# Kernel optimization log

Measured on AMD Instinct MI355X. Metric: run time of the kernel, lower is better.

Reference implementation:

```python
import jax, jax.numpy as jnp
import numpy as np

NUM_LAYERS = 4
INPUT_DIM = 512
BATCH = 16384


def setup_inputs() -> dict:
    key = jax.random.key(0)
    kx, kw, kb = jax.random.split(key, 3)
    x = jax.random.normal(kx, (BATCH, INPUT_DIM), dtype=jnp.float32)
    # PyTorch nn.Linear init: U(-1/sqrt(fan_in), 1/sqrt(fan_in))
    bound = 1.0 / np.sqrt(INPUT_DIM)
    W = jax.random.uniform(kw, (NUM_LAYERS, INPUT_DIM, INPUT_DIM), jnp.float32, -bound, bound)
    b = jax.random.uniform(kb, (NUM_LAYERS, INPUT_DIM), jnp.float32, -bound, bound)
    return {"x": x, "W": W, "b": b}


def reference(x, W, b):
    # x: [B, D]; W: [L, D, D] (torch Linear weight, so y = x @ W_i.T + b_i)
    x_list = [x]
    for i in range(NUM_LAYERS):
        x_ = x_list[-1]
        # sequentially accumulate dot-product residuals against all prior activations
        for x_pre in x_list[:-1]:
            s = jnp.sum(x_ * x_pre, axis=-1, keepdims=True)  # [B, 1]
            x_ = x_ + s
        y = jnp.einsum("bd,ed->be", x_, W[i]) + b[i]  # Linear: x_ @ W_i.T + b_i
        x_list.append(y)
    out = jnp.concatenate(x_list[1:], axis=-1)  # [B, L*D]
    return out
```

## Files before the change

kernel.cpp:

```cpp
#include <hip/hip_runtime.h>
#include <stdint.h>


#define BROWS 16384
#define DIM 512
#define NL 4
#define OUTSTRIDE (NL * DIM)

#define BM 128
#define BN 128
#define BK 32

typedef unsigned short ushort_t;
typedef __attribute__((ext_vector_type(8))) short bf16x8;
typedef __attribute__((ext_vector_type(4))) float f32x4;

__device__ inline ushort_t f32_to_bf16(float f) {
    union { float f; uint32_t u; } v; v.f = f;
    uint32_t u = v.u;
    uint32_t r = (u + 0x7fffu + ((u >> 16) & 1u)) >> 16;
    return (ushort_t)r;
}

__device__ inline float bf16_bits_to_f32(ushort_t u) {
    union { uint32_t u; float f; } v; v.u = ((uint32_t)u) << 16; return v.f;
}

__device__ inline float wave_reduce_sum(float v) {
    #pragma unroll
    for (int off = 32; off > 0; off >>= 1) v += __shfl_down(v, off, 64);
    return v;
}

__global__ __launch_bounds__(256) void convw_kernel(
    const float* __restrict__ W, ushort_t* __restrict__ Wb,
    float* __restrict__ wsum)
{
    int row = blockIdx.x;
    int t = threadIdx.x;
    const float* wp = W + (size_t)row * DIM;
    float f0 = wp[2 * t], f1 = wp[2 * t + 1];
    ushort_t* wbp = Wb + (size_t)row * DIM;
    wbp[2 * t]     = f32_to_bf16(f0);
    wbp[2 * t + 1] = f32_to_bf16(f1);
    __shared__ float red[4];
    int wave = t >> 6, lane = t & 63;
    float r = wave_reduce_sum(f0 + f1);
    if (lane == 0) red[wave] = r;
    __syncthreads();
    if (t == 0) wsum[row] = red[0] + red[1] + red[2] + red[3];
}

__global__ __launch_bounds__(256) void conv0_kernel(
    const float* __restrict__ x0, ushort_t* __restrict__ xb0,
    float* __restrict__ sums)
{
    int wave = threadIdx.x >> 6, lane = threadIdx.x & 63;
    int b = blockIdx.x * 4 + wave;
    const float* xp = x0 + (size_t)b * DIM + lane * 8;
    float4 a = ((const float4*)xp)[0];
    float4 c4 = ((const float4*)xp)[1];
    float f[8] = {a.x, a.y, a.z, a.w, c4.x, c4.y, c4.z, c4.w};
    bf16x8 o;
    float s = 0.f;
    #pragma unroll
    for (int i = 0; i < 8; ++i) {
        o[i] = (short)f32_to_bf16(f[i]);
        s += f[i];
    }
    *(bf16x8*)(xb0 + (size_t)b * DIM + lane * 8) = o;
    s = wave_reduce_sum(s);
    if (lane == 0) sums[b] = s;
}

__global__ __launch_bounds__(256) void dots_kernel(
    const ushort_t* __restrict__ xb, float* __restrict__ sums,
    float* __restrict__ cvals, int lp1)
{
    int wave = threadIdx.x >> 6, lane = threadIdx.x & 63;
    int b = blockIdx.x * 4 + wave;
    bf16x8 v = *(const bf16x8*)(xb + ((size_t)lp1 * BROWS + b) * DIM + lane * 8);
    float xi[8];
    float ssum = 0.f;
    #pragma unroll
    for (int i = 0; i < 8; ++i) {
        xi[i] = bf16_bits_to_f32((ushort_t)v[i]);
        ssum += xi[i];
    }
    float dots[3] = {0.f, 0.f, 0.f};
    #pragma unroll
    for (int j = 0; j < 3; ++j) {
        if (j < lp1) {
            bf16x8 w = *(const bf16x8*)(xb + ((size_t)j * BROWS + b) * DIM + lane * 8);
            float d = 0.f;
            #pragma unroll
            for (int i = 0; i < 8; ++i)
                d += xi[i] * bf16_bits_to_f32((ushort_t)w[i]);
            dots[j] = d;
        }
    }
    ssum = wave_reduce_sum(ssum);
    #pragma unroll
    for (int j = 0; j < 3; ++j)
        dots[j] = wave_reduce_sum(dots[j]);
    if (lane == 0) {
        sums[lp1 * BROWS + b] = ssum;
        float c = 0.f;
        for (int j = 0; j < lp1; ++j)
            c = c + dots[j] + c * sums[j * BROWS + b];
        cvals[lp1 * BROWS + b] = c;
    }
}

__global__ __launch_bounds__(256) void gemm_kernel(
    const ushort_t* __restrict__ A,
    const ushort_t* __restrict__ Wb,
    const float* __restrict__ bias,
    const float* __restrict__ wsum,
    const float* __restrict__ cvals,
    float* __restrict__ out,
    ushort_t* __restrict__ xb_next)
{
    __shared__ __align__(16) ushort_t sA[BM * BK];
    __shared__ __align__(16) ushort_t sB[BN * BK];

    int tid  = threadIdx.x;
    int wave = tid >> 6;
    int lane = tid & 63;
    int wm = wave >> 1, wn = wave & 1;
    int bm = blockIdx.y * BM;
    int bn = blockIdx.x * BN;

    f32x4 acc[4][4] = {};

    int srow = lane >> 2;
    int scol = (lane & 3) * 8;

    for (int k0 = 0; k0 < DIM; k0 += BK) {
        __syncthreads();
        #pragma unroll
        for (int t2 = 0; t2 < 2; ++t2) {
            int r = wave * 32 + t2 * 16;
            const ushort_t* gA = A  + (size_t)(bm + r + srow) * DIM + k0 + scol;
            const ushort_t* gB = Wb + (size_t)(bn + r + srow) * DIM + k0 + scol;
            __builtin_amdgcn_global_load_lds(
                (const __attribute__((address_space(1))) void*)gA,
                (__attribute__((address_space(3))) void*)(sA + r * BK), 16, 0, 0);
            __builtin_amdgcn_global_load_lds(
                (const __attribute__((address_space(1))) void*)gB,
                (__attribute__((address_space(3))) void*)(sB + r * BK), 16, 0, 0);
        }
        __syncthreads();

        int q = lane >> 4;
        int rr = lane & 15;
        bf16x8 af[4], bfr[4];
        #pragma unroll
        for (int mi = 0; mi < 4; ++mi)
            af[mi] = *(const bf16x8*)(sA + (wm * 64 + mi * 16 + rr) * BK + q * 8);
        #pragma unroll
        for (int ni = 0; ni < 4; ++ni)
            bfr[ni] = *(const bf16x8*)(sB + (wn * 64 + ni * 16 + rr) * BK + q * 8);
        #pragma unroll
        for (int mi = 0; mi < 4; ++mi)
            #pragma unroll
            for (int ni = 0; ni < 4; ++ni)
                acc[mi][ni] = __builtin_amdgcn_mfma_f32_16x16x32_bf16(
                    af[mi], bfr[ni], acc[mi][ni], 0, 0, 0);
    }

    int q = lane >> 4, nlane = lane & 15;
    #pragma unroll
    for (int ni = 0; ni < 4; ++ni) {
        int n_g = bn + wn * 64 + ni * 16 + nlane;
        float ws = wsum[n_g];
        float bs = bias[n_g];
        #pragma unroll
        for (int mi = 0; mi < 4; ++mi) {
            int m_base = bm + wm * 64 + mi * 16 + q * 4;
            #pragma unroll
            for (int r = 0; r < 4; ++r) {
                int m_g = m_base + r;
                float c = cvals ? cvals[m_g] : 0.f;
                float v = acc[mi][ni][r] + c * ws + bs;
                out[(size_t)m_g * OUTSTRIDE + n_g] = v;
                if (xb_next)
                    xb_next[(size_t)m_g * DIM + n_g] = f32_to_bf16(v);
            }
        }
    }
}

extern "C" void kernel_launch(void* const* d_in, const int* in_sizes, int n_in,
                              void* d_out, int out_size, void* d_ws, size_t ws_size,
                              hipStream_t stream) {
    (void)in_sizes; (void)n_in; (void)out_size; (void)ws_size;
    const float* x0   = (const float*)d_in[0];
    const float* W    = (const float*)d_in[1];
    const float* bias = (const float*)d_in[2];
    float* out = (float*)d_out;

    char* ws = (char*)d_ws;
    ushort_t* xb   = (ushort_t*)ws;
    ushort_t* Wb   = (ushort_t*)(ws + 67108864);
    float*    wsum = (float*)   (ws + 69206016);
    float*    sums = (float*)   (ws + 69214208);
    float*    cvals= (float*)   (ws + 69476352);

    convw_kernel<<<NL * DIM, 256, 0, stream>>>(W, Wb, wsum);
    conv0_kernel<<<BROWS / 4, 256, 0, stream>>>(x0, xb, sums);

    dim3 ggrid(DIM / BN, BROWS / BM);
    for (int l = 0; l < NL; ++l) {
        gemm_kernel<<<ggrid, 256, 0, stream>>>(
            xb + (size_t)l * BROWS * DIM,
            Wb + (size_t)l * DIM * DIM,
            bias + l * DIM,
            wsum + l * DIM,
            (l > 0) ? (cvals + l * BROWS) : nullptr,
            out + l * DIM,
            (l < NL - 1) ? (xb + (size_t)(l + 1) * BROWS * DIM) : nullptr);
        if (l < NL - 1)
            dots_kernel<<<BROWS / 4, 256, 0, stream>>>(xb, sums, cvals, l + 1);
    }
}
```

Before: 302.8 us.

## Fuse dot-product reductions into GEMM epilogue, double-buffer LDS, merge prep kernels

```diff
diff --git a/kernel.cpp b/kernel.cpp
--- a/kernel.cpp
+++ b/kernel.cpp
@@ -10,6 +10,7 @@
 #define BM 128
 #define BN 128
 #define BK 32
+#define NT (DIM / BK)
 
 typedef unsigned short ushort_t;
 typedef __attribute__((ext_vector_type(8))) short bf16x8;
@@ -32,160 +33,191 @@
     return v;
 }
 
-__global__ __launch_bounds__(256) void convw_kernel(
-    const float* __restrict__ W, ushort_t* __restrict__ Wb,
-    float* __restrict__ wsum)
+__global__ __launch_bounds__(256) void prep_kernel(
+    const float* __restrict__ W, const float* __restrict__ x0,
+    ushort_t* __restrict__ Wb, float* __restrict__ wsum,
+    ushort_t* __restrict__ xb0, float* __restrict__ sum0)
 {
-    int row = blockIdx.x;
     int t = threadIdx.x;
-    const float* wp = W + (size_t)row * DIM;
-    float f0 = wp[2 * t], f1 = wp[2 * t + 1];
-    ushort_t* wbp = Wb + (size_t)row * DIM;
-    wbp[2 * t]     = f32_to_bf16(f0);
-    wbp[2 * t + 1] = f32_to_bf16(f1);
-    __shared__ float red[4];
     int wave = t >> 6, lane = t & 63;
-    float r = wave_reduce_sum(f0 + f1);
-    if (lane == 0) red[wave] = r;
-    __syncthreads();
-    if (t == 0) wsum[row] = red[0] + red[1] + red[2] + red[3];
-}
-
-__global__ __launch_bounds__(256) void conv0_kernel(
-    const float* __restrict__ x0, ushort_t* __restrict__ xb0,
-    float* __restrict__ sums)
-{
-    int wave = threadIdx.x >> 6, lane = threadIdx.x & 63;
-    int b = blockIdx.x * 4 + wave;
-    const float* xp = x0 + (size_t)b * DIM + lane * 8;
-    float4 a = ((const float4*)xp)[0];
-    float4 c4 = ((const float4*)xp)[1];
-    float f[8] = {a.x, a.y, a.z, a.w, c4.x, c4.y, c4.z, c4.w};
-    bf16x8 o;
-    float s = 0.f;
-    #pragma unroll
-    for (int i = 0; i < 8; ++i) {
-        o[i] = (short)f32_to_bf16(f[i]);
-        s += f[i];
-    }
-    *(bf16x8*)(xb0 + (size_t)b * DIM + lane * 8) = o;
-    s = wave_reduce_sum(s);
-    if (lane == 0) sums[b] = s;
-}
-
-__global__ __launch_bounds__(256) void dots_kernel(
-    const ushort_t* __restrict__ xb, float* __restrict__ sums,
-    float* __restrict__ cvals, int lp1)
-{
-    int wave = threadIdx.x >> 6, lane = threadIdx.x & 63;
-    int b = blockIdx.x * 4 + wave;
-    bf16x8 v = *(const bf16x8*)(xb + ((size_t)lp1 * BROWS + b) * DIM + lane * 8);
-    float xi[8];
-    float ssum = 0.f;
-    #pragma unroll
-    for (int i = 0; i < 8; ++i) {
-        xi[i] = bf16_bits_to_f32((ushort_t)v[i]);
-        ssum += xi[i];
-    }
-    float dots[3] = {0.f, 0.f, 0.f};
-    #pragma unroll
-    for (int j = 0; j < 3; ++j) {
-        if (j < lp1) {
-            bf16x8 w = *(const bf16x8*)(xb + ((size_t)j * BROWS + b) * DIM + lane * 8);
-            float d = 0.f;
-            #pragma unroll
-            for (int i = 0; i < 8; ++i)
-                d += xi[i] * bf16_bits_to_f32((ushort_t)w[i]);
-            dots[j] = d;
-        }
-    }
-    ssum = wave_reduce_sum(ssum);
-    #pragma unroll
-    for (int j = 0; j < 3; ++j)
-        dots[j] = wave_reduce_sum(dots[j]);
-    if (lane == 0) {
-        sums[lp1 * BROWS + b] = ssum;
-        float c = 0.f;
-        for (int j = 0; j < lp1; ++j)
-            c = c + dots[j] + c * sums[j * BROWS + b];
-        cvals[lp1 * BROWS + b] = c;
-    }
-}
-
+    if (blockIdx.x < NL * DIM) {
+        int row = blockIdx.x;
+        const float* wp = W + (size_t)row * DIM;
+        float f0 = wp[2 * t], f1 = wp[2 * t + 1];
+        ushort_t* wbp = Wb + (size_t)row * DIM;
+        wbp[2 * t]     = f32_to_bf16(f0);
+        wbp[2 * t + 1] = f32_to_bf16(f1);
+        __shared__ float red[4];
+        float r = wave_reduce_sum(f0 + f1);
+        if (lane == 0) red[wave] = r;
+        __syncthreads();
+        if (t == 0) wsum[row] = red[0] + red[1] + red[2] + red[3];
+    } else {
+        int b = (blockIdx.x - NL * DIM) * 4 + wave;
+        const float* xp = x0 + (size_t)b * DIM + lane * 8;
+        float4 a = ((const float4*)xp)[0];
+        float4 c4 = ((const float4*)xp)[1];
+        float f[8] = {a.x, a.y, a.z, a.w, c4.x, c4.y, c4.z, c4.w};
+        bf16x8 o;
+        float s = 0.f;
+        #pragma unroll
+        for (int i = 0; i < 8; ++i) {
+            o[i] = (short)f32_to_bf16(f[i]);
+            s += f[i];
+        }
+        *(bf16x8*)(xb0 + (size_t)b * DIM + lane * 8) = o;
+        s = wave_reduce_sum(s);
+        if (lane == 0) sum0[b] = s;
+    }
+}
+
+template <int L, bool HASNEXT>
 __global__ __launch_bounds__(256) void gemm_kernel(
-    const ushort_t* __restrict__ A,
+    const ushort_t* __restrict__ xb,
     const ushort_t* __restrict__ Wb,
     const float* __restrict__ bias,
     const float* __restrict__ wsum,
-    const float* __restrict__ cvals,
     float* __restrict__ out,
-    ushort_t* __restrict__ xb_next)
+    ushort_t* __restrict__ xb_next,
+    const float* __restrict__ sum0,
+    float* __restrict__ psum,
+    float* __restrict__ pdot)
 {
-    __shared__ __align__(16) ushort_t sA[BM * BK];
-    __shared__ __align__(16) ushort_t sB[BN * BK];
+    __shared__ __align__(16) ushort_t sA[2][BM * BK];
+    __shared__ __align__(16) ushort_t sB[2][BN * BK];
+    __shared__ float sC[BM];
 
     int tid  = threadIdx.x;
     int wave = tid >> 6;
     int lane = tid & 63;
     int wm = wave >> 1, wn = wave & 1;
-    int bm = blockIdx.y * BM;
-    int bn = blockIdx.x * BN;
+
+    int lid  = blockIdx.x;
+    int xcd  = lid & 7, slot = lid >> 3;
+    int orig = xcd * 64 + slot;
+    int bx = orig & 3, by = orig >> 2;
+    int bm = by * BM;
+    int bn = bx * BN;
+
+    const ushort_t* A = xb + (size_t)L * BROWS * DIM;
 
     f32x4 acc[4][4] = {};
 
     int srow = lane >> 2;
     int scol = (lane & 3) * 8;
-
-    for (int k0 = 0; k0 < DIM; k0 += BK) {
-        __syncthreads();
+    const ushort_t* gA0 = A  + (size_t)(bm + srow) * DIM + scol;
+    const ushort_t* gB0 = Wb + (size_t)(bn + srow) * DIM + scol;
+
+    auto stage = [&](int buf, int k0) {
         #pragma unroll
         for (int t2 = 0; t2 < 2; ++t2) {
             int r = wave * 32 + t2 * 16;
-            const ushort_t* gA = A  + (size_t)(bm + r + srow) * DIM + k0 + scol;
-            const ushort_t* gB = Wb + (size_t)(bn + r + srow) * DIM + k0 + scol;
             __builtin_amdgcn_global_load_lds(
-                (const __attribute__((address_space(1))) void*)gA,
-                (__attribute__((address_space(3))) void*)(sA + r * BK), 16, 0, 0);
+                (const __attribute__((address_space(1))) void*)(gA0 + (size_t)r * DIM + k0),
+                (__attribute__((address_space(3))) void*)(&sA[buf][r * BK]), 16, 0, 0);
             __builtin_amdgcn_global_load_lds(
-                (const __attribute__((address_space(1))) void*)gB,
-                (__attribute__((address_space(3))) void*)(sB + r * BK), 16, 0, 0);
-        }
-        __syncthreads();
-
-        int q = lane >> 4;
-        int rr = lane & 15;
+                (const __attribute__((address_space(1))) void*)(gB0 + (size_t)r * DIM + k0),
+                (__attribute__((address_space(3))) void*)(&sB[buf][r * BK]), 16, 0, 0);
+        }
+    };
+
+    stage(0, 0);
+    __syncthreads();
+
+    int q8 = (lane >> 4) * 8;
+    int rr = lane & 15;
+    for (int t = 0; t < NT; ++t) {
+        int cur = t & 1;
+        if (t + 1 < NT) stage(cur ^ 1, (t + 1) * BK);
         bf16x8 af[4], bfr[4];
         #pragma unroll
         for (int mi = 0; mi < 4; ++mi)
-            af[mi] = *(const bf16x8*)(sA + (wm * 64 + mi * 16 + rr) * BK + q * 8);
+            af[mi] = *(const bf16x8*)(&sA[cur][(wm * 64 + mi * 16 + rr) * BK + q8]);
         #pragma unroll
         for (int ni = 0; ni < 4; ++ni)
-            bfr[ni] = *(const bf16x8*)(sB + (wn * 64 + ni * 16 + rr) * BK + q * 8);
+            bfr[ni] = *(const bf16x8*)(&sB[cur][(wn * 64 + ni * 16 + rr) * BK + q8]);
         #pragma unroll
         for (int mi = 0; mi < 4; ++mi)
             #pragma unroll
             for (int ni = 0; ni < 4; ++ni)
                 acc[mi][ni] = __builtin_amdgcn_mfma_f32_16x16x32_bf16(
                     af[mi], bfr[ni], acc[mi][ni], 0, 0, 0);
+        __syncthreads();
+    }
+
+    if (L > 0) {
+        if (tid < BM) {
+            int row = bm + tid;
+            float c = 0.f;
+            #pragma unroll
+            for (int j = 0; j < L; ++j) {
+                constexpr int pb = L * (L - 1) / 2;
+                const float* pd = pdot + ((size_t)(pb + j) * 8) * BROWS + row;
+                float d = 0.f;
+                #pragma unroll
+                for (int p = 0; p < 8; ++p) d += pd[(size_t)p * BROWS];
+                float sj;
+                if (j == 0) sj = sum0[row];
+                else {
+                    const float* ps = psum + ((size_t)(j - 1) * 8) * BROWS + row;
+                    sj = 0.f;
+                    #pragma unroll
+                    for (int p = 0; p < 8; ++p) sj += ps[(size_t)p * BROWS];
+                }
+                c = c + d + c * sj;
+            }
+            sC[tid] = c;
+        }
+        __syncthreads();
     }
 
     int q = lane >> 4, nlane = lane & 15;
+    int pq = wn * 4 + bx;
+    float ws4[4], bs4[4];
     #pragma unroll
     for (int ni = 0; ni < 4; ++ni) {
         int n_g = bn + wn * 64 + ni * 16 + nlane;
-        float ws = wsum[n_g];
-        float bs = bias[n_g];
-        #pragma unroll
-        for (int mi = 0; mi < 4; ++mi) {
-            int m_base = bm + wm * 64 + mi * 16 + q * 4;
+        ws4[ni] = wsum[n_g];
+        bs4[ni] = bias[n_g];
+    }
+    #pragma unroll
+    for (int mi = 0; mi < 4; ++mi) {
+        #pragma unroll
+        for (int r = 0; r < 4; ++r) {
+            int mloc = wm * 64 + mi * 16 + q * 4 + r;
+            int m_g = bm + mloc;
+            float c = (L > 0) ? sC[mloc] : 0.f;
+            float vsum = 0.f, vdot0 = 0.f, vdot1 = 0.f, vdot2 = 0.f;
             #pragma unroll
-            for (int r = 0; r < 4; ++r) {
-                int m_g = m_base + r;
-                float c = cvals ? cvals[m_g] : 0.f;
-                float v = acc[mi][ni][r] + c * ws + bs;
+            for (int ni = 0; ni < 4; ++ni) {
+                int n_g = bn + wn * 64 + ni * 16 + nlane;
+                float v = acc[mi][ni][r] + c * ws4[ni] + bs4[ni];
                 out[(size_t)m_g * OUTSTRIDE + n_g] = v;
-                if (xb_next)
+                if constexpr (HASNEXT) {
                     xb_next[(size_t)m_g * DIM + n_g] = f32_to_bf16(v);
+                    vsum += v;
+                    vdot0 += v * bf16_bits_to_f32(xb[((size_t)0 * BROWS + m_g) * DIM + n_g]);
+                    if (L >= 1)
+                        vdot1 += v * bf16_bits_to_f32(xb[((size_t)1 * BROWS + m_g) * DIM + n_g]);
+                    if (L >= 2)
+                        vdot2 += v * bf16_bits_to_f32(xb[((size_t)2 * BROWS + m_g) * DIM + n_g]);
+                }
+            }
+            if constexpr (HASNEXT) {
+                #pragma unroll
+                for (int off = 8; off > 0; off >>= 1) {
+                    vsum  += __shfl_xor(vsum,  off, 64);
+                    vdot0 += __shfl_xor(vdot0, off, 64);
+                    if (L >= 1) vdot1 += __shfl_xor(vdot1, off, 64);
+                    if (L >= 2) vdot2 += __shfl_xor(vdot2, off, 64);
+                }
+                if (nlane == 0) {
+                    constexpr int pbn = (L + 1) * L / 2;
+                    psum[((size_t)L * 8 + pq) * BROWS + m_g] = vsum;
+                    pdot[((size_t)(pbn + 0) * 8 + pq) * BROWS + m_g] = vdot0;
+                    if (L >= 1) pdot[((size_t)(pbn + 1) * 8 + pq) * BROWS + m_g] = vdot1;
+                    if (L >= 2) pdot[((size_t)(pbn + 2) * 8 + pq) * BROWS + m_g] = vdot2;
+                }
             }
         }
     }
@@ -204,23 +236,23 @@
     ushort_t* xb   = (ushort_t*)ws;
     ushort_t* Wb   = (ushort_t*)(ws + 67108864);
     float*    wsum = (float*)   (ws + 69206016);
-    float*    sums = (float*)   (ws + 69214208);
-    float*    cvals= (float*)   (ws + 69476352);
-
-    convw_kernel<<<NL * DIM, 256, 0, stream>>>(W, Wb, wsum);
-    conv0_kernel<<<BROWS / 4, 256, 0, stream>>>(x0, xb, sums);
-
-    dim3 ggrid(DIM / BN, BROWS / BM);
-    for (int l = 0; l < NL; ++l) {
-        gemm_kernel<<<ggrid, 256, 0, stream>>>(
-            xb + (size_t)l * BROWS * DIM,
-            Wb + (size_t)l * DIM * DIM,
-            bias + l * DIM,
-            wsum + l * DIM,
-            (l > 0) ? (cvals + l * BROWS) : nullptr,
-            out + l * DIM,
-            (l < NL - 1) ? (xb + (size_t)(l + 1) * BROWS * DIM) : nullptr);
-        if (l < NL - 1)
-            dots_kernel<<<BROWS / 4, 256, 0, stream>>>(xb, sums, cvals, l + 1);
-    }
-}
+    float*    sum0 = (float*)   (ws + 69214208);
+    float*    psum = (float*)   (ws + 69279744);
+    float*    pdot = (float*)   (ws + 70852608);
+
+    prep_kernel<<<NL * DIM + BROWS / 4, 256, 0, stream>>>(W, x0, Wb, wsum, xb, sum0);
+
+    const int nblk = (BROWS / BM) * (DIM / BN);
+    gemm_kernel<0, true><<<nblk, 256, 0, stream>>>(
+        xb, Wb, bias, wsum, out,
+        xb + (size_t)1 * BROWS * DIM, sum0, psum, pdot);
+    gemm_kernel<1, true><<<nblk, 256, 0, stream>>>(
+        xb, Wb + (size_t)1 * DIM * DIM, bias + DIM, wsum + DIM, out + DIM,
+        xb + (size_t)2 * BROWS * DIM, sum0, psum, pdot);
+    gemm_kernel<2, true><<<nblk, 256, 0, stream>>>(
+        xb, Wb + (size_t)2 * DIM * DIM, bias + 2 * DIM, wsum + 2 * DIM, out + 2 * DIM,
+        xb + (size_t)3 * BROWS * DIM, sum0, psum, pdot);
+    gemm_kernel<3, false><<<nblk, 256, 0, stream>>>(
+        xb, Wb + (size_t)3 * DIM * DIM, bias + 3 * DIM, wsum + 3 * DIM, out + 3 * DIM,
+        nullptr, sum0, psum, pdot);
+}
```

After: 257.4 us. 15.0% less time.

## Fuse all four cross layers into one persistent row-block kernel with LDS-resident activations

Applied to the files above, without the earlier changes.

```diff
diff --git a/kernel.cpp b/kernel.cpp
--- a/kernel.cpp
+++ b/kernel.cpp
@@ -7,9 +7,10 @@
 #define NL 4
 #define OUTSTRIDE (NL * DIM)
 
-#define BM 128
-#define BN 128
+#define BM 64
 #define BK 32
+#define SEG (DIM / BK)
+#define NSTEP (NL * SEG)
 
 typedef unsigned short ushort_t;
 typedef __attribute__((ext_vector_type(8))) short bf16x8;
@@ -22,8 +23,11 @@
     return (ushort_t)r;
 }
 
-__device__ inline float bf16_bits_to_f32(ushort_t u) {
-    union { uint32_t u; float f; } v; v.u = ((uint32_t)u) << 16; return v.f;
+__device__ inline float bf16_lo(uint32_t p) {
+    union { uint32_t u; float f; } v; v.u = p << 16; return v.f;
+}
+__device__ inline float bf16_hi(uint32_t p) {
+    union { uint32_t u; float f; } v; v.u = p & 0xffff0000u; return v.f;
 }
 
 __device__ inline float wave_reduce_sum(float v) {
@@ -32,7 +36,7 @@
     return v;
 }
 
-__global__ __launch_bounds__(256) void convw_kernel(
+__global__ __launch_bounds__(256) void prep_kernel(
     const float* __restrict__ W, ushort_t* __restrict__ Wb,
     float* __restrict__ wsum)
 {
@@ -51,142 +55,221 @@
     if (t == 0) wsum[row] = red[0] + red[1] + red[2] + red[3];
 }
 
-__global__ __launch_bounds__(256) void conv0_kernel(
-    const float* __restrict__ x0, ushort_t* __restrict__ xb0,
-    float* __restrict__ sums)
-{
-    int wave = threadIdx.x >> 6, lane = threadIdx.x & 63;
-    int b = blockIdx.x * 4 + wave;
-    const float* xp = x0 + (size_t)b * DIM + lane * 8;
-    float4 a = ((const float4*)xp)[0];
-    float4 c4 = ((const float4*)xp)[1];
-    float f[8] = {a.x, a.y, a.z, a.w, c4.x, c4.y, c4.z, c4.w};
-    bf16x8 o;
-    float s = 0.f;
-    #pragma unroll
-    for (int i = 0; i < 8; ++i) {
-        o[i] = (short)f32_to_bf16(f[i]);
-        s += f[i];
-    }
-    *(bf16x8*)(xb0 + (size_t)b * DIM + lane * 8) = o;
-    s = wave_reduce_sum(s);
-    if (lane == 0) sums[b] = s;
-}
-
-__global__ __launch_bounds__(256) void dots_kernel(
-    const ushort_t* __restrict__ xb, float* __restrict__ sums,
-    float* __restrict__ cvals, int lp1)
-{
-    int wave = threadIdx.x >> 6, lane = threadIdx.x & 63;
-    int b = blockIdx.x * 4 + wave;
-    bf16x8 v = *(const bf16x8*)(xb + ((size_t)lp1 * BROWS + b) * DIM + lane * 8);
-    float xi[8];
-    float ssum = 0.f;
-    #pragma unroll
-    for (int i = 0; i < 8; ++i) {
-        xi[i] = bf16_bits_to_f32((ushort_t)v[i]);
-        ssum += xi[i];
-    }
-    float dots[3] = {0.f, 0.f, 0.f};
-    #pragma unroll
-    for (int j = 0; j < 3; ++j) {
-        if (j < lp1) {
-            bf16x8 w = *(const bf16x8*)(xb + ((size_t)j * BROWS + b) * DIM + lane * 8);
-            float d = 0.f;
-            #pragma unroll
-            for (int i = 0; i < 8; ++i)
-                d += xi[i] * bf16_bits_to_f32((ushort_t)w[i]);
-            dots[j] = d;
-        }
-    }
-    ssum = wave_reduce_sum(ssum);
-    #pragma unroll
-    for (int j = 0; j < 3; ++j)
-        dots[j] = wave_reduce_sum(dots[j]);
-    if (lane == 0) {
-        sums[lp1 * BROWS + b] = ssum;
-        float c = 0.f;
-        for (int j = 0; j < lp1; ++j)
-            c = c + dots[j] + c * sums[j * BROWS + b];
-        cvals[lp1 * BROWS + b] = c;
-    }
-}
-
-__global__ __launch_bounds__(256) void gemm_kernel(
-    const ushort_t* __restrict__ A,
+__global__ __launch_bounds__(512, 1) void cross_kernel(
+    const float* __restrict__ x0,
     const ushort_t* __restrict__ Wb,
     const float* __restrict__ bias,
     const float* __restrict__ wsum,
-    const float* __restrict__ cvals,
-    float* __restrict__ out,
-    ushort_t* __restrict__ xb_next)
+    float* __restrict__ out)
 {
-    __shared__ __align__(16) ushort_t sA[BM * BK];
-    __shared__ __align__(16) ushort_t sB[BN * BK];
+    __shared__ __align__(16) ushort_t sAct[BM * DIM];
+    __shared__ __align__(16) ushort_t sB[2][DIM * BK];
+    __shared__ float sRed[4][4][BM];
+    __shared__ float sSums[4][BM];
+    __shared__ float sCn[BM];
 
     int tid  = threadIdx.x;
     int wave = tid >> 6;
     int lane = tid & 63;
-    int wm = wave >> 1, wn = wave & 1;
-    int bm = blockIdx.y * BM;
-    int bn = blockIdx.x * BN;
-
-    f32x4 acc[4][4] = {};
-
-    int srow = lane >> 2;
-    int scol = (lane & 3) * 8;
-
-    for (int k0 = 0; k0 < DIM; k0 += BK) {
-        __syncthreads();
-        #pragma unroll
-        for (int t2 = 0; t2 < 2; ++t2) {
-            int r = wave * 32 + t2 * 16;
-            const ushort_t* gA = A  + (size_t)(bm + r + srow) * DIM + k0 + scol;
-            const ushort_t* gB = Wb + (size_t)(bn + r + srow) * DIM + k0 + scol;
+    int wm  = wave >> 2;
+    int wn4 = wave & 3;
+    int q = lane >> 4;
+    int rr = lane & 15;
+    int nlane = lane & 15;
+    int bm = blockIdx.x * BM;
+
+    int beoff[4];
+    #pragma unroll
+    for (int j = 0; j < 4; ++j) {
+        int brow = wave * 64 + j * 16 + (lane >> 2);
+        int chunk = (lane & 3) ^ (brow & 3);
+        beoff[j] = brow * DIM + chunk * 8;
+    }
+
+    auto stageB = [&](int s) {
+        int cur = s & 1;
+        const ushort_t* base = Wb + ((size_t)(s >> 4) * DIM + (size_t)((s & 15) * BK) / DIM) * DIM;
+        const ushort_t* gb = Wb + (size_t)(s >> 4) * DIM * DIM + (s & 15) * BK;
+        (void)base;
+        #pragma unroll
+        for (int j = 0; j < 4; ++j) {
             __builtin_amdgcn_global_load_lds(
-                (const __attribute__((address_space(1))) void*)gA,
-                (__attribute__((address_space(3))) void*)(sA + r * BK), 16, 0, 0);
-            __builtin_amdgcn_global_load_lds(
-                (const __attribute__((address_space(1))) void*)gB,
-                (__attribute__((address_space(3))) void*)(sB + r * BK), 16, 0, 0);
-        }
-        __syncthreads();
-
-        int q = lane >> 4;
-        int rr = lane & 15;
-        bf16x8 af[4], bfr[4];
-        #pragma unroll
-        for (int mi = 0; mi < 4; ++mi)
-            af[mi] = *(const bf16x8*)(sA + (wm * 64 + mi * 16 + rr) * BK + q * 8);
-        #pragma unroll
-        for (int ni = 0; ni < 4; ++ni)
-            bfr[ni] = *(const bf16x8*)(sB + (wn * 64 + ni * 16 + rr) * BK + q * 8);
-        #pragma unroll
-        for (int mi = 0; mi < 4; ++mi)
-            #pragma unroll
-            for (int ni = 0; ni < 4; ++ni)
-                acc[mi][ni] = __builtin_amdgcn_mfma_f32_16x16x32_bf16(
-                    af[mi], bfr[ni], acc[mi][ni], 0, 0, 0);
+                (const __attribute__((address_space(1))) void*)(gb + beoff[j]),
+                (__attribute__((address_space(3))) void*)(&sB[cur][(wave * 64 + j * 16) * BK]),
+                16, 0, 0);
+        }
+    };
+
+    stageB(0);
+    stageB(1);
+
+    #pragma unroll
+    for (int r8 = 0; r8 < 8; ++r8) {
+        int row = wave * 8 + r8;
+        const float* xp = x0 + (size_t)(bm + row) * DIM + lane * 8;
+        float4 a = ((const float4*)xp)[0];
+        float4 b4 = ((const float4*)xp)[1];
+        float f[8] = {a.x, a.y, a.z, a.w, b4.x, b4.y, b4.z, b4.w};
+        bf16x8 o;
+        float s = 0.f;
+        #pragma unroll
+        for (int i = 0; i < 8; ++i) { o[i] = (short)f32_to_bf16(f[i]); s += f[i]; }
+        int kc = lane ^ (row & 7);
+        *(bf16x8*)(&sAct[row * DIM + kc * 8]) = o;
+        s = wave_reduce_sum(s);
+        if (lane == 0) sSums[0][row] = s;
     }
-
-    int q = lane >> 4, nlane = lane & 15;
-    #pragma unroll
-    for (int ni = 0; ni < 4; ++ni) {
-        int n_g = bn + wn * 64 + ni * 16 + nlane;
-        float ws = wsum[n_g];
-        float bs = bias[n_g];
-        #pragma unroll
-        for (int mi = 0; mi < 4; ++mi) {
-            int m_base = bm + wm * 64 + mi * 16 + q * 4;
+    __syncthreads();
+
+    uint32_t vk0[32], vk1[32], vk2[32];
+
+    #pragma unroll
+    for (int l = 0; l < NL; ++l) {
+        f32x4 acc[2][8] = {};
+
+        for (int t = 0; t < SEG; ++t) {
+            int s = l * SEG + t;
+            int cur = s & 1;
+            if (s < NSTEP - 1) { asm volatile("s_waitcnt vmcnt(4)" ::: "memory"); }
+            else               { asm volatile("s_waitcnt vmcnt(0)" ::: "memory"); }
+            __builtin_amdgcn_s_barrier();
+            __builtin_amdgcn_sched_barrier(0);
+
+            bf16x8 af[2], bfr[8];
+            #pragma unroll
+            for (int mi = 0; mi < 2; ++mi) {
+                int arow = wm * 32 + mi * 16 + rr;
+                int kc = (t * 4 + q) ^ (arow & 7);
+                af[mi] = *(const bf16x8*)(&sAct[arow * DIM + kc * 8]);
+            }
+            int ch2 = q ^ (rr & 3);
+            #pragma unroll
+            for (int ni = 0; ni < 8; ++ni) {
+                int erow = wn4 * 128 + ni * 16 + rr;
+                bfr[ni] = *(const bf16x8*)(&sB[cur][erow * BK + ch2 * 8]);
+            }
+            asm volatile("s_waitcnt lgkmcnt(0)" ::: "memory");
+            __builtin_amdgcn_sched_barrier(0);
+            __builtin_amdgcn_s_barrier();
+            if (s + 2 < NSTEP) stageB(s + 2);
+
+            #pragma unroll
+            for (int mi = 0; mi < 2; ++mi)
+                #pragma unroll
+                for (int ni = 0; ni < 8; ++ni)
+                    acc[mi][ni] = __builtin_amdgcn_mfma_f32_16x16x32_bf16(
+                        af[mi], bfr[ni], acc[mi][ni], 0, 0, 0);
+        }
+
+        float ws8[8], bs8[8];
+        #pragma unroll
+        for (int ni = 0; ni < 8; ++ni) {
+            int ng = wn4 * 128 + ni * 16 + nlane;
+            ws8[ni] = wsum[l * DIM + ng];
+            bs8[ni] = bias[l * DIM + ng];
+        }
+        float cl8[8];
+        #pragma unroll
+        for (int mi = 0; mi < 2; ++mi)
+            #pragma unroll
+            for (int r = 0; r < 4; ++r)
+                cl8[mi * 4 + r] = (l == 0) ? 0.f : sCn[wm * 32 + mi * 16 + q * 4 + r];
+
+        if (l == 0) {
+            #pragma unroll
+            for (int mi = 0; mi < 2; ++mi)
+                #pragma unroll
+                for (int r = 0; r < 4; ++r) {
+                    int row = wm * 32 + mi * 16 + q * 4 + r;
+                    #pragma unroll
+                    for (int nip = 0; nip < 4; ++nip) {
+                        int kc0 = (wn4 * 16 + 4 * nip + (nlane >> 3)) ^ (row & 7);
+                        int kc1 = (wn4 * 16 + 4 * nip + 2 + (nlane >> 3)) ^ (row & 7);
+                        uint32_t b0 = sAct[row * DIM + kc0 * 8 + (nlane & 7)];
+                        uint32_t b1 = sAct[row * DIM + kc1 * 8 + (nlane & 7)];
+                        vk0[(mi * 4 + r) * 4 + nip] = b0 | (b1 << 16);
+                    }
+                }
+            asm volatile("s_waitcnt lgkmcnt(0)" ::: "memory");
+        }
+
+        #pragma unroll
+        for (int mi = 0; mi < 2; ++mi)
             #pragma unroll
             for (int r = 0; r < 4; ++r) {
-                int m_g = m_base + r;
-                float c = cvals ? cvals[m_g] : 0.f;
-                float v = acc[mi][ni][r] + c * ws + bs;
-                out[(size_t)m_g * OUTSTRIDE + n_g] = v;
-                if (xb_next)
-                    xb_next[(size_t)m_g * DIM + n_g] = f32_to_bf16(v);
-            }
+                int mr = mi * 4 + r;
+                int row = wm * 32 + mi * 16 + q * 4 + r;
+                float cc = cl8[mr];
+                float vv[8];
+                #pragma unroll
+                for (int ni = 0; ni < 8; ++ni) {
+                    vv[ni] = acc[mi][ni][r] + cc * ws8[ni] + bs8[ni];
+                    int colg = wn4 * 128 + ni * 16 + nlane;
+                    out[(size_t)(bm + row) * OUTSTRIDE + l * DIM + colg] = vv[ni];
+                }
+                if (l < 3) {
+                    float vs = 0.f, d0 = 0.f, d1 = 0.f, d2 = 0.f;
+                    #pragma unroll
+                    for (int ni = 0; ni < 8; ++ni) vs += vv[ni];
+                    #pragma unroll
+                    for (int nip = 0; nip < 4; ++nip) {
+                        uint32_t p0 = vk0[mr * 4 + nip];
+                        d0 += vv[2 * nip] * bf16_lo(p0) + vv[2 * nip + 1] * bf16_hi(p0);
+                        if (l >= 1) {
+                            uint32_t p1 = vk1[mr * 4 + nip];
+                            d1 += vv[2 * nip] * bf16_lo(p1) + vv[2 * nip + 1] * bf16_hi(p1);
+                        }
+                        if (l >= 2) {
+                            uint32_t p2 = vk2[mr * 4 + nip];
+                            d2 += vv[2 * nip] * bf16_lo(p2) + vv[2 * nip + 1] * bf16_hi(p2);
+                        }
+                    }
+                    #pragma unroll
+                    for (int nip = 0; nip < 4; ++nip) {
+                        ushort_t h0 = f32_to_bf16(vv[2 * nip]);
+                        ushort_t h1 = f32_to_bf16(vv[2 * nip + 1]);
+                        int kc0 = (wn4 * 16 + 4 * nip + (nlane >> 3)) ^ (row & 7);
+                        int kc1 = (wn4 * 16 + 4 * nip + 2 + (nlane >> 3)) ^ (row & 7);
+                        sAct[row * DIM + kc0 * 8 + (nlane & 7)] = h0;
+                        sAct[row * DIM + kc1 * 8 + (nlane & 7)] = h1;
+                        uint32_t pk = (uint32_t)h0 | ((uint32_t)h1 << 16);
+                        if (l == 0) vk1[mr * 4 + nip] = pk;
+                        if (l == 1) vk2[mr * 4 + nip] = pk;
+                    }
+                    #pragma unroll
+                    for (int off = 8; off > 0; off >>= 1) {
+                        vs += __shfl_xor(vs, off, 64);
+                        d0 += __shfl_xor(d0, off, 64);
+                        if (l >= 1) d1 += __shfl_xor(d1, off, 64);
+                        if (l >= 2) d2 += __shfl_xor(d2, off, 64);
+                    }
+                    if (nlane == 0) {
+                        sRed[0][wn4][row] = vs;
+                        sRed[1][wn4][row] = d0;
+                        if (l >= 1) sRed[2][wn4][row] = d1;
+                        if (l >= 2) sRed[3][wn4][row] = d2;
+                    }
+                }
+            }
+
+        if (l < 3) {
+            __syncthreads();
+            if (tid < BM) {
+                float vs = sRed[0][0][tid] + sRed[0][1][tid] + sRed[0][2][tid] + sRed[0][3][tid];
+                float d0 = sRed[1][0][tid] + sRed[1][1][tid] + sRed[1][2][tid] + sRed[1][3][tid];
+                float c = d0;
+                if (l >= 1) {
+                    float d1 = sRed[2][0][tid] + sRed[2][1][tid] + sRed[2][2][tid] + sRed[2][3][tid];
+                    c = c + d1 + c * sSums[1][tid];
+                }
+                if (l >= 2) {
+                    float d2 = sRed[3][0][tid] + sRed[3][1][tid] + sRed[3][2][tid] + sRed[3][3][tid];
+                    c = c + d2 + c * sSums[2][tid];
+                }
+                sCn[tid] = c;
+                sSums[l + 1][tid] = vs;
+            }
+            __syncthreads();
         }
     }
 }
@@ -201,26 +284,9 @@
     float* out = (float*)d_out;
 
     char* ws = (char*)d_ws;
-    ushort_t* xb   = (ushort_t*)ws;
-    ushort_t* Wb   = (ushort_t*)(ws + 67108864);
-    float*    wsum = (float*)   (ws + 69206016);
-    float*    sums = (float*)   (ws + 69214208);
-    float*    cvals= (float*)   (ws + 69476352);
-
-    convw_kernel<<<NL * DIM, 256, 0, stream>>>(W, Wb, wsum);
-    conv0_kernel<<<BROWS / 4, 256, 0, stream>>>(x0, xb, sums);
-
-    dim3 ggrid(DIM / BN, BROWS / BM);
-    for (int l = 0; l < NL; ++l) {
-        gemm_kernel<<<ggrid, 256, 0, stream>>>(
-            xb + (size_t)l * BROWS * DIM,
-            Wb + (size_t)l * DIM * DIM,
-            bias + l * DIM,
-            wsum + l * DIM,
-            (l > 0) ? (cvals + l * BROWS) : nullptr,
-            out + l * DIM,
-            (l < NL - 1) ? (xb + (size_t)(l + 1) * BROWS * DIM) : nullptr);
-        if (l < NL - 1)
-            dots_kernel<<<BROWS / 4, 256, 0, stream>>>(xb, sums, cvals, l + 1);
-    }
-}
+    ushort_t* Wb   = (ushort_t*)ws;
+    float*    wsum = (float*)(ws + 2097152);
+
+    prep_kernel<<<NL * DIM, 256, 0, stream>>>(W, Wb, wsum);
+    cross_kernel<<<BROWS / BM, 512, 0, stream>>>(x0, Wb, bias, wsum, out);
+}
```

Result: faster. 290.3 us (-4.1%).
